# Kernel tuning notes

Measured on AMD Instinct MI355X. Metric: run time of the kernel, lower is better.

Reference implementation:

```python
import jax, jax.numpy as jnp
import numpy as np

N = 50000   # nodes
E = 800000  # edges (avg degree 16)
G = 64      # graphs in batch

def _lin(k, fi, fo):
    kw, kb = jax.random.split(k)
    s = 1.0 / np.sqrt(fi)
    w = jax.random.uniform(kw, (fi, fo), minval=-s, maxval=s, dtype=jnp.float32)
    b = jax.random.uniform(kb, (fo,), minval=-s, maxval=s, dtype=jnp.float32)
    return w, b

def setup_inputs():
    key = jax.random.key(0)
    ks = jax.random.split(key, 12)
    pos = jax.random.normal(ks[0], (N, 3), dtype=jnp.float32)
    edge_index = jax.random.randint(ks[1], (2, E), 0, N, dtype=jnp.int32)
    batch = jnp.sort(jax.random.randint(ks[2], (N,), 0, G, dtype=jnp.int32))
    w_proj, b_proj = _lin(ks[3], 3, 64)
    # message passing layers: self-weight, neighbor-weight, bias
    ws0, bb0 = _lin(ks[4], 64, 64);  wn0, _ = _lin(jax.random.fold_in(ks[4], 1), 64, 64)
    ws1, bb1 = _lin(ks[5], 64, 64);  wn1, _ = _lin(jax.random.fold_in(ks[5], 1), 64, 64)
    ws2, bb2 = _lin(ks[6], 64, 128); wn2, _ = _lin(jax.random.fold_in(ks[6], 1), 64, 128)
    ws3, bb3 = _lin(ks[7], 256, 256); wn3, _ = _lin(jax.random.fold_in(ks[7], 1), 256, 256)
    # dense head: concat(max, mean) = 512 -> 512 -> 256
    wd1, bd1 = _lin(ks[8], 512, 512)
    wd2, bd2 = _lin(ks[9], 512, 256)
    return {"pos": pos, "edge_index": edge_index, "batch": batch,
            "w_proj": w_proj, "b_proj": b_proj,
            "ws0": ws0, "wn0": wn0, "bb0": bb0,
            "ws1": ws1, "wn1": wn1, "bb1": bb1,
            "ws2": ws2, "wn2": wn2, "bb2": bb2,
            "ws3": ws3, "wn3": wn3, "bb3": bb3,
            "wd1": wd1, "bd1": bd1, "wd2": wd2, "bd2": bd2}

def reference(pos, edge_index, batch, w_proj, b_proj,
              ws0, wn0, bb0, ws1, wn1, bb1, ws2, wn2, bb2, ws3, wn3, bb3,
              wd1, bd1, wd2, bd2):
    src, dst = edge_index[0], edge_index[1]
    x = pos @ w_proj + b_proj  # node projection [N,64]
    # in-degree counts, computed once
    deg = jnp.maximum(
        jax.ops.segment_sum(jnp.ones((E, 1), x.dtype), dst, num_segments=N), 1.0)

    def mp(h, ws, wn, b):
        # mean-aggregate neighbor messages: gather on src, scatter-add on dst
        agg = jax.ops.segment_sum(h[src], dst, num_segments=N) / deg
        return jax.nn.leaky_relu(h @ ws + agg @ wn + b)

    h0 = mp(x, ws0, wn0, bb0)   # [N,64]
    h1 = mp(h0, ws1, wn1, bb1)  # [N,64]
    h2 = mp(h1, ws2, wn2, bb2)  # [N,128]
    nf = mp(jnp.concatenate([h0, h1, h2], axis=-1), ws3, wn3, bb3)  # [N,256]

    # scatter max/mean pooling over graph ids
    gcnt = jnp.maximum(
        jax.ops.segment_sum(jnp.ones((N, 1), nf.dtype), batch, num_segments=G), 1.0)
    x1 = jax.ops.segment_max(nf, batch, num_segments=G)
    x2 = jax.ops.segment_sum(nf, batch, num_segments=G) / gcnt
    g = jnp.concatenate([x1, x2], axis=-1)  # [G,512]

    g = jax.nn.leaky_relu(g @ wd1 + bd1)
    return g @ wd2 + bd2  # [G,256]
```

## Files before the change

### kernel.cpp

```cpp
#include <hip/hip_runtime.h>
#include <math.h>

typedef _Float16 f16x8 __attribute__((ext_vector_type(8)));
typedef unsigned short us8 __attribute__((ext_vector_type(8)));
typedef float f32x4 __attribute__((ext_vector_type(4)));

__device__ inline unsigned short f2h(float f) {
    _Float16 h = (_Float16)f;
    return *(unsigned short*)&h;
}
__device__ inline float h2f(unsigned short u) {
    _Float16 h = *(_Float16*)&u;
    return (float)h;
}

__device__ __forceinline__ size_t pkoff(int row, int col, int KT) {
    return ((size_t)(row >> 4) * (KT >> 5) + (col >> 5)) * 512
         + (size_t)(((col >> 3) & 3) * 128 + ((row & 15) << 3) + (col & 7));
}

#define ECH 4096

__global__ __launch_bounds__(256)
void bucket_hist(const int* __restrict__ edst, int* __restrict__ bcnt, int E, int NB) {
    __shared__ int h[512];
    int tid = threadIdx.x;
    for (int i = tid; i < NB; i += 256) h[i] = 0;
    __syncthreads();
    int c0 = blockIdx.x * ECH, c1 = min(c0 + ECH, E);
    for (int e = c0 + tid; e < c1; e += 256) atomicAdd(&h[edst[e] >> 7], 1);
    __syncthreads();
    for (int i = tid; i < NB; i += 256) if (h[i]) atomicAdd(&bcnt[i], h[i]);
}

__global__ __launch_bounds__(512)
void bucket_scan(const int* __restrict__ bcnt, int* __restrict__ bbase,
                 int* __restrict__ bcur, int* __restrict__ rowstart, int NB, int n) {
    __shared__ int ws[8];
    int tid = threadIdx.x, lane = tid & 63, wid = tid >> 6;
    int v = (tid < NB) ? bcnt[tid] : 0;
    int x = v;
    for (int d = 1; d < 64; d <<= 1) { int y = __shfl_up(x, d); if (lane >= d) x += y; }
    if (lane == 63) ws[wid] = x;
    __syncthreads();
    int off = 0;
    for (int w = 0; w < wid; w++) off += ws[w];
    int excl = x - v + off;
    if (tid < NB) { bbase[tid] = excl; bcur[tid] = excl; }
    if (tid == 0) {
        int tot = 0;
        for (int w = 0; w < 8; w++) tot += ws[w];
        bbase[NB] = tot;
        rowstart[n] = tot;
    }
}

__global__ __launch_bounds__(256)
void bucket_scatter(const int* __restrict__ esrc_in, const int* __restrict__ edst_in,
                    int* __restrict__ bcur, unsigned* __restrict__ bedge, int E, int NB) {
    __shared__ int h[512];
    __shared__ int rb[512];
    int tid = threadIdx.x;
    for (int i = tid; i < NB; i += 256) h[i] = 0;
    __syncthreads();
    int c0 = blockIdx.x * ECH, c1 = min(c0 + ECH, E);
    for (int e = c0 + tid; e < c1; e += 256) atomicAdd(&h[edst_in[e] >> 7], 1);
    __syncthreads();
    for (int i = tid; i < NB; i += 256) {
        rb[i] = h[i] ? atomicAdd(&bcur[i], h[i]) : 0;
        h[i] = 0;
    }
    __syncthreads();
    for (int e = c0 + tid; e < c1; e += 256) {
        int dst = edst_in[e], src = esrc_in[e];
        int b = dst >> 7;
        int o = atomicAdd(&h[b], 1);
        bedge[rb[b] + o] = (unsigned)src | ((unsigned)(dst & 127) << 16);
    }
}

__global__ __launch_bounds__(256)
void node_csr(const unsigned* __restrict__ bedge, const int* __restrict__ bbase,
              int* __restrict__ rowstart, float* __restrict__ degf,
              unsigned short* __restrict__ esrc, int n) {
    __shared__ int cnt[128];
    __shared__ int cur[128];
    __shared__ int ws4[4];
    int b = blockIdx.x, tid = threadIdx.x;
    int lane = tid & 63, wid = tid >> 6;
    int n0 = b << 7;
    int eb0 = bbase[b], eb1 = bbase[b + 1];
    if (tid < 128) cnt[tid] = 0;
    __syncthreads();
    for (int e = eb0 + tid; e < eb1; e += 256) atomicAdd(&cnt[(bedge[e] >> 16) & 127], 1);
    __syncthreads();
    int v = (tid < 128) ? cnt[tid] : 0;
    int x = v;
    for (int d = 1; d < 64; d <<= 1) { int y = __shfl_up(x, d); if (lane >= d) x += y; }
    if (lane == 63) ws4[wid] = x;
    __syncthreads();
    int off = 0;
    for (int w = 0; w < wid; w++) off += ws4[w];
    int excl = x - v + off;
    if (tid < 128 && n0 + tid < n) {
        rowstart[n0 + tid] = eb0 + excl;
        cur[tid] = eb0 + excl;
        degf[n0 + tid] = (float)(v > 0 ? v : 1);
    }
    __syncthreads();
    for (int e = eb0 + tid; e < eb1; e += 256) {
        unsigned u = bedge[e];
        int p = atomicAdd(&cur[(u >> 16) & 127], 1);
        esrc[p] = (unsigned short)(u & 0xffffu);
    }
}

__global__ __launch_bounds__(256)
void wcvt_pk(const float* __restrict__ Ws, const float* __restrict__ Wn,
             int K2, int FOUT, unsigned short* __restrict__ out) {
    int t = blockIdx.x * 256 + threadIdx.x;
    int total = 2 * K2 * FOUT;
    if (t >= total) return;
    int k = t / FOUT, n = t - k * FOUT;
    float v = (k < K2) ? Ws[k * FOUT + n] : Wn[(k - K2) * FOUT + n];
    out[pkoff(n, k, 2 * K2)] = f2h(v);
}

__global__ __launch_bounds__(256)
void proj_k(const float* __restrict__ pos, const float* __restrict__ w,
            const float* __restrict__ b, unsigned short* __restrict__ XB0row,
            unsigned short* __restrict__ XB0pk, int n_nodes) {
    int t = blockIdx.x * 256 + threadIdx.x;
    int n = t >> 6, f = t & 63;
    if (n >= n_nodes) return;
    float p0 = pos[n * 3 + 0], p1 = pos[n * 3 + 1], p2 = pos[n * 3 + 2];
    float v = b[f] + p0 * w[f] + p1 * w[64 + f] + p2 * w[128 + f];
    unsigned short h = f2h(v);
    XB0row[(size_t)n * 128 + f] = h;
    XB0pk[pkoff(n, f, 128)] = h;
}

template <int F, int KT>
__global__ __launch_bounds__(256)
void agg_pk(const unsigned short* __restrict__ src, int sstr,
            unsigned short* __restrict__ dpk, int dc,
            const int* __restrict__ rowstart, const unsigned short* __restrict__ esrc,
            const float* __restrict__ degf, int n_nodes) {
    int wave = threadIdx.x >> 6;
    int lane = threadIdx.x & 63;
    int n = blockIdx.x * 4 + wave;
    if (n >= n_nodes) return;
    const int ST = (F == 64) ? 2 : 1;
    int half = (F == 64) ? (lane >> 5) : 0;
    int li   = (F == 64) ? (lane & 31) : lane;
    int e0 = rowstart[n], e1 = rowstart[n + 1];
    float a0 = 0.f, a1 = 0.f;
    int e = e0 + half;
    for (; e + 3 * ST < e1; e += 4 * ST) {
        int s0 = esrc[e], s1 = esrc[e + ST], s2 = esrc[e + 2 * ST], s3 = esrc[e + 3 * ST];
        unsigned p0 = *(const unsigned*)&src[(size_t)s0 * sstr + 2 * li];
        unsigned p1 = *(const unsigned*)&src[(size_t)s1 * sstr + 2 * li];
        unsigned p2 = *(const unsigned*)&src[(size_t)s2 * sstr + 2 * li];
        unsigned p3 = *(const unsigned*)&src[(size_t)s3 * sstr + 2 * li];
        a0 += h2f((unsigned short)(p0 & 0xffffu)) + h2f((unsigned short)(p1 & 0xffffu))
            + h2f((unsigned short)(p2 & 0xffffu)) + h2f((unsigned short)(p3 & 0xffffu));
        a1 += h2f((unsigned short)(p0 >> 16)) + h2f((unsigned short)(p1 >> 16))
            + h2f((unsigned short)(p2 >> 16)) + h2f((unsigned short)(p3 >> 16));
    }
    for (; e < e1; e += ST) {
        int s = esrc[e];
        unsigned p = *(const unsigned*)&src[(size_t)s * sstr + 2 * li];
        a0 += h2f((unsigned short)(p & 0xffffu));
        a1 += h2f((unsigned short)(p >> 16));
    }
    if (F == 64) { a0 += __shfl_xor(a0, 32); a1 += __shfl_xor(a1, 32); }
    float inv = 1.0f / degf[n];
    unsigned out = (unsigned)f2h(a0 * inv) | ((unsigned)f2h(a1 * inv) << 16);
    if (F != 64 || lane < 32) {
        int c = dc + 2 * li;
        *(unsigned*)&dpk[pkoff(n, c, KT)] = out;
    }
}

__device__ inline void atomicMaxFloat(float* addr, float v) {
    if (v >= 0.f) atomicMax((int*)addr, __float_as_int(v));
    else          atomicMin((unsigned int*)addr, __float_as_uint(v));
}

template <int K, int KTA, int MT, int NTB, int POOL>
__global__ __launch_bounds__(64)
void gemm_fr(const unsigned short* __restrict__ Apk, int KA1, int ac1, int ac2,
             const unsigned short* __restrict__ Wpk, const float* __restrict__ bias,
             unsigned short* __restrict__ Drow, int dcol,
             unsigned short* __restrict__ Dpk, int KTD,
             float* __restrict__ pmax, float* __restrict__ psum,
             const int* __restrict__ batch, int M) {
    const int NS = K / 32;
    __shared__ unsigned short tile[MT * 16][NTB * 16 + 8];
    __shared__ int bsh[MT * 16];
    int lane = threadIdx.x;
    int lm = lane & 15, kb = lane >> 4;
    int rb0 = blockIdx.x * MT;
    int nb0 = blockIdx.y * NTB;
    int m0 = rb0 * 16;

    if (POOL) {
        if (lane < MT * 16) {
            int gm = m0 + lane;
            bsh[lane] = batch[gm < M ? gm : (M - 1)];
        }
        __syncthreads();
    }

    f32x4 acc[MT][NTB] = {};

    auto loadf = [&](f16x8* A_, f16x8* B_, int s) {
        int kk = s * 32;
        int phys = (kk < KA1) ? (ac1 + kk) : (ac2 + (kk - KA1));
        size_t ak = (size_t)(phys >> 5) * 512 + (size_t)lane * 8;
        #pragma unroll
        for (int mf = 0; mf < MT; mf++)
            A_[mf] = *(const f16x8*)&Apk[(size_t)(rb0 + mf) * (KTA / 32) * 512 + ak];
        #pragma unroll
        for (int nt = 0; nt < NTB; nt++)
            B_[nt] = *(const f16x8*)&Wpk[((size_t)(nb0 + nt) * (K / 32) + s) * 512 + (size_t)lane * 8];
    };
    auto domfma = [&](f16x8* A_, f16x8* B_) {
        #pragma unroll
        for (int nt = 0; nt < NTB; nt++)
            #pragma unroll
            for (int mf = 0; mf < MT; mf++)
                acc[mf][nt] = __builtin_amdgcn_mfma_f32_16x16x32_f16(A_[mf], B_[nt], acc[mf][nt], 0, 0, 0);
    };

    f16x8 aA[MT], bA[NTB], aB[MT], bB[NTB];
    loadf(aA, bA, 0);
    for (int s = 0; s < NS; s += 2) {
        loadf(aB, bB, s + 1);
        domfma(aA, bA);
        if (s + 2 < NS) loadf(aA, bA, s + 2);
        domfma(aB, bB);
    }

    if (!POOL) {
        #pragma unroll
        for (int nt = 0; nt < NTB; nt++) {
            int colL = nt * 16 + lm;
            float bv = bias[nb0 * 16 + colL];
            #pragma unroll
            for (int mf = 0; mf < MT; mf++) {
                #pragma unroll
                for (int r = 0; r < 4; r++) {
                    float v = acc[mf][nt][r] + bv;
                    v = (v > 0.f) ? v : 0.01f * v;
                    unsigned short h = f2h(v);
                    tile[mf * 16 + kb * 4 + r][colL] = h;
                    int gm = m0 + mf * 16 + kb * 4 + r;
                    if (gm < M) Drow[(size_t)gm * 256 + dcol + nb0 * 16 + colL] = h;
                }
            }
        }
        __syncthreads();
        int dkg0 = (dcol + nb0 * 16) >> 5;
        #pragma unroll
        for (int mf = 0; mf < MT; mf++) {
            #pragma unroll
            for (int kg = 0; kg < NTB / 2; kg++) {
                us8 u = *(const us8*)&tile[mf * 16 + lm][kg * 32 + kb * 8];
                *(us8*)&Dpk[((size_t)(rb0 + mf) * (KTD / 32) + dkg0 + kg) * 512 + (size_t)lane * 8] = u;
            }
        }
    } else {
        bool uni = (bsh[0] == bsh[MT * 16 - 1]);
        if (uni) {
            int g = bsh[0];
            #pragma unroll
            for (int nt = 0; nt < NTB; nt++) {
                int col = (nb0 + nt) * 16 + lm;
                float bv = bias[col];
                float mx = -INFINITY, sm = 0.f;
                #pragma unroll
                for (int mf = 0; mf < MT; mf++) {
                    #pragma unroll
                    for (int r = 0; r < 4; r++) {
                        int gm = m0 + mf * 16 + kb * 4 + r;
                        if (gm >= M) continue;
                        float v = acc[mf][nt][r] + bv;
                        v = (v > 0.f) ? v : 0.01f * v;
                        mx = fmaxf(mx, v); sm += v;
                    }
                }
                mx = fmaxf(mx, __shfl_xor(mx, 16));
                mx = fmaxf(mx, __shfl_xor(mx, 32));
                sm += __shfl_xor(sm, 16);
                sm += __shfl_xor(sm, 32);
                if (kb == 0 && mx > -INFINITY) {
                    atomicMaxFloat(&pmax[g * 256 + col], mx);
                    atomicAdd(&psum[g * 256 + col], sm);
                }
            }
        } else {
            #pragma unroll
            for (int nt = 0; nt < NTB; nt++) {
                int col = (nb0 + nt) * 16 + lm;
                float bv = bias[col];
                int curg = -1; float mx = -INFINITY, sm = 0.f;
                #pragma unroll
                for (int mf = 0; mf < MT; mf++) {
                    #pragma unroll
                    for (int r = 0; r < 4; r++) {
                        int gm = m0 + mf * 16 + kb * 4 + r;
                        if (gm >= M) continue;
                        int g = bsh[mf * 16 + kb * 4 + r];
                        if (g != curg) {
                            if (curg >= 0) {
                                atomicMaxFloat(&pmax[curg * 256 + col], mx);
                                atomicAdd(&psum[curg * 256 + col], sm);
                            }
                            curg = g; mx = -INFINITY; sm = 0.f;
                        }
                        float v = acc[mf][nt][r] + bv;
                        v = (v > 0.f) ? v : 0.01f * v;
                        mx = fmaxf(mx, v); sm += v;
                    }
                }
                if (curg >= 0) {
                    atomicMaxFloat(&pmax[curg * 256 + col], mx);
                    atomicAdd(&psum[curg * 256 + col], sm);
                }
            }
        }
    }
}

template <int K, int FOUT>
__global__ __launch_bounds__(256)
void gemm_lrelu(const float* __restrict__ A1, int a1s, int a1c, int KA1,
                const float* __restrict__ A2, int a2s, int a2c,
                const float* __restrict__ W1, const float* __restrict__ W2,
                const float* __restrict__ bias,
                float* __restrict__ D, int dstr, int dcol, int M, int doRelu) {
    const int BM = 64, BN = 64, BK = 16;
    __shared__ float As[BK][BM];
    __shared__ float Bs[BK][BN];
    int tid = threadIdx.x;
    int m0 = blockIdx.x * BM;
    int n0 = blockIdx.y * BN;
    int tx = tid & 15;
    int ty = tid >> 4;
    float acc[4][4] = {};
    int mA = tid >> 2;
    int kA = (tid & 3) * 4;
    int kB = tid >> 4;
    int nB = (tid & 15) * 4;
    for (int k0 = 0; k0 < K; k0 += BK) {
        int kk = k0 + kA;
        const float* Ap; int Asr; int Acc;
        if (kk < KA1) { Ap = A1; Asr = a1s; Acc = a1c + kk; }
        else          { Ap = A2; Asr = a2s; Acc = a2c + (kk - KA1); }
        int gm = m0 + mA;
        float4 av;
        if (gm < M) av = *(const float4*)&Ap[(size_t)gm * Asr + Acc];
        else        av = float4{0.f, 0.f, 0.f, 0.f};
        As[kA + 0][mA] = av.x; As[kA + 1][mA] = av.y;
        As[kA + 2][mA] = av.z; As[kA + 3][mA] = av.w;
        int kw = k0 + kB;
        const float* Wp; int kwl;
        if (kw < K / 2) { Wp = W1; kwl = kw; } else { Wp = W2; kwl = kw - K / 2; }
        float4 bv = *(const float4*)&Wp[(size_t)kwl * FOUT + n0 + nB];
        *(float4*)&Bs[kB][nB] = bv;
        __syncthreads();
        #pragma unroll
        for (int k = 0; k < BK; k++) {
            float a[4], b[4];
            *(float4*)a = *(const float4*)&As[k][ty * 4];
            *(float4*)b = *(const float4*)&Bs[k][tx * 4];
            #pragma unroll
            for (int i = 0; i < 4; i++)
                #pragma unroll
                for (int j = 0; j < 4; j++)
                    acc[i][j] += a[i] * b[j];
        }
        __syncthreads();
    }
    #pragma unroll
    for (int i = 0; i < 4; i++) {
        int gm = m0 + ty * 4 + i;
        if (gm >= M) continue;
        #pragma unroll
        for (int j = 0; j < 4; j++) {
            int gn = n0 + tx * 4 + j;
            float v = acc[i][j] + bias[gn];
            if (doRelu) v = (v > 0.f) ? v : 0.01f * v;
            D[(size_t)gm * dstr + dcol + gn] = v;
        }
    }
}

__global__ __launch_bounds__(256)
void pool_init(float* __restrict__ pmax, float* __restrict__ psum, int G) {
    int t = blockIdx.x * 256 + threadIdx.x;
    if (t < G * 256) { pmax[t] = -INFINITY; psum[t] = 0.f; }
}

__global__ __launch_bounds__(256)
void pool_final(const float* __restrict__ pmax, const float* __restrict__ psum,
                const int* __restrict__ batch, float* __restrict__ pooled,
                int G, int n_nodes) {
    int t = blockIdx.x * 256 + threadIdx.x;
    if (t >= G * 256) return;
    int g = t >> 8, f = t & 255;
    int lo = 0, hi = n_nodes;
    while (lo < hi) { int mid = (lo + hi) >> 1; if (batch[mid] < g) lo = mid + 1; else hi = mid; }
    int start = lo;
    lo = start; hi = n_nodes;
    while (lo < hi) { int mid = (lo + hi) >> 1; if (batch[mid] < g + 1) lo = mid + 1; else hi = mid; }
    int end = lo;
    int c = end - start;
    float mx = pmax[t];
    if (c == 0) mx = 0.f;
    pooled[g * 512 + f] = mx;
    pooled[g * 512 + 256 + f] = psum[t] / (float)(c > 0 ? c : 1);
}

extern "C" void kernel_launch(void* const* d_in, const int* in_sizes, int n_in,
                              void* d_out, int out_size, void* d_ws, size_t ws_size,
                              hipStream_t stream) {
    const float* pos   = (const float*)d_in[0];
    const int*   eidx  = (const int*)d_in[1];
    const int*   batch = (const int*)d_in[2];
    const float* w_proj = (const float*)d_in[3];
    const float* b_proj = (const float*)d_in[4];
    const float* ws0 = (const float*)d_in[5];  const float* wn0 = (const float*)d_in[6];  const float* bb0 = (const float*)d_in[7];
    const float* ws1 = (const float*)d_in[8];  const float* wn1 = (const float*)d_in[9];  const float* bb1 = (const float*)d_in[10];
    const float* ws2 = (const float*)d_in[11]; const float* wn2 = (const float*)d_in[12]; const float* bb2 = (const float*)d_in[13];
    const float* ws3 = (const float*)d_in[14]; const float* wn3 = (const float*)d_in[15]; const float* bb3 = (const float*)d_in[16];
    const float* wd1 = (const float*)d_in[17]; const float* bd1 = (const float*)d_in[18];
    const float* wd2 = (const float*)d_in[19]; const float* bd2 = (const float*)d_in[20];

    int N = in_sizes[0] / 3;
    int E = in_sizes[1] / 2;
    int G = out_size / 256;
    const int* esrc_in = eidx;
    const int* edst_in = eidx + E;

    int NRB = (N + 15) / 16 + 1;
    int NB  = (N + 127) >> 7;

    char* base = (char*)d_ws;
    size_t off = 0;
    auto alloc = [&](size_t bytes) -> void* {
        void* p = base + off;
        off = (off + bytes + 255) & ~(size_t)255;
        return p;
    };
    int*   rowstart = (int*)alloc((size_t)(N + 1) * 4);
    float* degf     = (float*)alloc((size_t)N * 4);
    int*   bcnt     = (int*)alloc((size_t)512 * 4);
    int*   bbase    = (int*)alloc((size_t)513 * 4);
    int*   bcur     = (int*)alloc((size_t)512 * 4);
    unsigned* bedge = (unsigned*)alloc((size_t)E * 4);
    unsigned short* esrc = (unsigned short*)alloc((size_t)E * 2);
    unsigned short* XB0row = (unsigned short*)alloc((size_t)N * 128 * 2);
    unsigned short* XB0pk  = (unsigned short*)alloc((size_t)NRB * 16 * 128 * 2);
    unsigned short* XBrow  = (unsigned short*)alloc((size_t)N * 256 * 2);
    unsigned short* XBpk   = (unsigned short*)alloc((size_t)NRB * 16 * 512 * 2);
    float* pooled   = (float*)alloc((size_t)G * 512 * 4);
    float* hid      = (float*)alloc((size_t)G * 512 * 4);
    float* pmax     = (float*)alloc((size_t)G * 256 * 4);
    float* psum     = (float*)alloc((size_t)G * 256 * 4);
    unsigned short* WP0 = (unsigned short*)alloc((size_t)64 * 128 * 2);
    unsigned short* WP1 = (unsigned short*)alloc((size_t)64 * 128 * 2);
    unsigned short* WP2 = (unsigned short*)alloc((size_t)128 * 128 * 2);
    unsigned short* WP3 = (unsigned short*)alloc((size_t)256 * 512 * 2);

    wcvt_pk<<<(2 * 64 * 64 + 255) / 256, 256, 0, stream>>>(ws0, wn0, 64, 64, WP0);
    wcvt_pk<<<(2 * 64 * 64 + 255) / 256, 256, 0, stream>>>(ws1, wn1, 64, 64, WP1);
    wcvt_pk<<<(2 * 64 * 128 + 255) / 256, 256, 0, stream>>>(ws2, wn2, 64, 128, WP2);
    wcvt_pk<<<(2 * 256 * 256 + 255) / 256, 256, 0, stream>>>(ws3, wn3, 256, 256, WP3);

    (void)hipMemsetAsync(bcnt, 0, (size_t)512 * 4, stream);
    int eb = (E + ECH - 1) / ECH;
    bucket_hist<<<eb, 256, 0, stream>>>(edst_in, bcnt, E, NB);
    bucket_scan<<<1, 512, 0, stream>>>(bcnt, bbase, bcur, rowstart, NB, N);
    bucket_scatter<<<eb, 256, 0, stream>>>(esrc_in, edst_in, bcur, bedge, E, NB);
    node_csr<<<NB, 256, 0, stream>>>(bedge, bbase, rowstart, degf, esrc, N);

    proj_k<<<(N * 64 + 255) / 256, 256, 0, stream>>>(pos, w_proj, b_proj, XB0row, XB0pk, N);

    int ab = (N + 3) / 4;
    int gb = (N + 31) / 32;

    agg_pk<64, 128><<<ab, 256, 0, stream>>>(XB0row, 128, XB0pk, 64, rowstart, esrc, degf, N);
    gemm_fr<128, 128, 2, 4, 0><<<dim3(gb, 1), 64, 0, stream>>>(
        XB0pk, 128, 0, 0, WP0, bb0, XBrow, 0, XBpk, 512, nullptr, nullptr, nullptr, N);

    agg_pk<64, 512><<<ab, 256, 0, stream>>>(XBrow, 256, XBpk, 256, rowstart, esrc, degf, N);
    gemm_fr<128, 512, 2, 4, 0><<<dim3(gb, 1), 64, 0, stream>>>(
        XBpk, 64, 0, 256, WP1, bb1, XBrow, 64, XBpk, 512, nullptr, nullptr, nullptr, N);

    agg_pk<64, 512><<<ab, 256, 0, stream>>>(XBrow + 64, 256, XBpk, 320, rowstart, esrc, degf, N);
    gemm_fr<128, 512, 2, 4, 0><<<dim3(gb, 2), 64, 0, stream>>>(
        XBpk, 64, 64, 320, WP2, bb2, XBrow, 128, XBpk, 512, nullptr, nullptr, nullptr, N);

    agg_pk<128, 512><<<ab, 256, 0, stream>>>(XBrow + 128, 256, XBpk, 384, rowstart, esrc, degf, N);
    pool_init<<<(G * 256 + 255) / 256, 256, 0, stream>>>(pmax, psum, G);
    gemm_fr<512, 512, 2, 8, 1><<<dim3(gb, 2), 64, 0, stream>>>(
        XBpk, 512, 0, 0, WP3, bb3, nullptr, 0, nullptr, 512, pmax, psum, batch, N);
    pool_final<<<(G * 256 + 255) / 256, 256, 0, stream>>>(pmax, psum, batch, pooled, G, N);

    gemm_lrelu<512, 512><<<dim3((G + 63) / 64, 8), 256, 0, stream>>>(
        pooled, 512, 0, 512, pooled, 512, 0, wd1, wd1 + 256 * 512, bd1, hid, 512, 0, G, 1);
    gemm_lrelu<512, 256><<<dim3((G + 63) / 64, 4), 256, 0, stream>>>(
        hid, 512, 0, 512, hid, 512, 0, wd2, wd2 + 256 * 256, bd2, (float*)d_out, 256, 0, G, 0);
}
```

Baseline: 319.6 us.

## Pack four waves per GEMM block and deepen A-fragment prefetch pipeline

The fragment GEMM now runs four independent wavefronts per 256-thread block, each taking its own 32-row stripe with a private LDS tile, so no block-wide barriers are needed. The K loop is fully unrolled with a 6-deep register ring buffer for A fragments and a 2-deep one for B, so more global loads are in flight ahead of the MFMAs. The pooling variant reads batch ids straight from global memory instead of staging them in shared memory. Register pressure rises with the deeper buffers and could reduce occupancy, and the padded row-block count grows to cover the larger grid granularity.

```diff
diff --git a/kernel.cpp b/kernel.cpp
--- a/kernel.cpp
+++ b/kernel.cpp
@@ -188,7 +188,7 @@
 }
 
 template <int K, int KTA, int MT, int NTB, int POOL>
-__global__ __launch_bounds__(64)
+__global__ __launch_bounds__(256)
 void gemm_fr(const unsigned short* __restrict__ Apk, int KA1, int ac1, int ac2,
              const unsigned short* __restrict__ Wpk, const float* __restrict__ bias,
              unsigned short* __restrict__ Drow, int dcol,
@@ -196,50 +196,52 @@
              float* __restrict__ pmax, float* __restrict__ psum,
              const int* __restrict__ batch, int M) {
     const int NS = K / 32;
-    __shared__ unsigned short tile[MT * 16][NTB * 16 + 8];
-    __shared__ int bsh[MT * 16];
-    int lane = threadIdx.x;
+    const int AD = (NS < 6) ? NS : 6;
+    const int BD = (NS < 2) ? NS : 2;
+    const int TSZ = POOL ? 4 : (MT * 16) * (NTB * 16 + 8);
+    __shared__ unsigned short tile_s[4][TSZ];
+    int w = threadIdx.x >> 6;
+    int lane = threadIdx.x & 63;
     int lm = lane & 15, kb = lane >> 4;
-    int rb0 = blockIdx.x * MT;
+    int rb0 = (blockIdx.x * 4 + w) * MT;
     int nb0 = blockIdx.y * NTB;
     int m0 = rb0 * 16;
-
-    if (POOL) {
-        if (lane < MT * 16) {
-            int gm = m0 + lane;
-            bsh[lane] = batch[gm < M ? gm : (M - 1)];
-        }
-        __syncthreads();
-    }
+    if (m0 >= M) return;
+    unsigned short* tile = tile_s[w];
 
     f32x4 acc[MT][NTB] = {};
-
-    auto loadf = [&](f16x8* A_, f16x8* B_, int s) {
+    f16x8 Ab[AD][MT];
+    f16x8 Bb[BD][NTB];
+
+    auto loadA = [&](int slot, int s) {
         int kk = s * 32;
         int phys = (kk < KA1) ? (ac1 + kk) : (ac2 + (kk - KA1));
         size_t ak = (size_t)(phys >> 5) * 512 + (size_t)lane * 8;
         #pragma unroll
         for (int mf = 0; mf < MT; mf++)
-            A_[mf] = *(const f16x8*)&Apk[(size_t)(rb0 + mf) * (KTA / 32) * 512 + ak];
+            Ab[slot][mf] = *(const f16x8*)&Apk[(size_t)(rb0 + mf) * (KTA / 32) * 512 + ak];
+    };
+    auto loadB = [&](int slot, int s) {
         #pragma unroll
         for (int nt = 0; nt < NTB; nt++)
-            B_[nt] = *(const f16x8*)&Wpk[((size_t)(nb0 + nt) * (K / 32) + s) * 512 + (size_t)lane * 8];
+            Bb[slot][nt] = *(const f16x8*)&Wpk[((size_t)(nb0 + nt) * (K / 32) + s) * 512 + (size_t)lane * 8];
     };
-    auto domfma = [&](f16x8* A_, f16x8* B_) {
+
+    #pragma unroll
+    for (int p = 0; p < AD; p++) loadA(p, p);
+    #pragma unroll
+    for (int p = 0; p < BD; p++) loadB(p, p);
+
+    #pragma unroll
+    for (int s = 0; s < NS; s++) {
         #pragma unroll
         for (int nt = 0; nt < NTB; nt++)
             #pragma unroll
             for (int mf = 0; mf < MT; mf++)
-                acc[mf][nt] = __builtin_amdgcn_mfma_f32_16x16x32_f16(A_[mf], B_[nt], acc[mf][nt], 0, 0, 0);
-    };
-
-    f16x8 aA[MT], bA[NTB], aB[MT], bB[NTB];
-    loadf(aA, bA, 0);
-    for (int s = 0; s < NS; s += 2) {
-        loadf(aB, bB, s + 1);
-        domfma(aA, bA);
-        if (s + 2 < NS) loadf(aA, bA, s + 2);
-        domfma(aB, bB);
+                acc[mf][nt] = __builtin_amdgcn_mfma_f32_16x16x32_f16(
+                    Ab[s % AD][mf], Bb[s % BD][nt], acc[mf][nt], 0, 0, 0);
+        if (s + BD < NS) loadB(s % BD, s + BD);
+        if (s + AD < NS) loadA(s % AD, s + AD);
     }
 
     if (!POOL) {
@@ -254,26 +256,34 @@
                     float v = acc[mf][nt][r] + bv;
                     v = (v > 0.f) ? v : 0.01f * v;
                     unsigned short h = f2h(v);
-                    tile[mf * 16 + kb * 4 + r][colL] = h;
+                    tile[(mf * 16 + kb * 4 + r) * (NTB * 16 + 8) + colL] = h;
                     int gm = m0 + mf * 16 + kb * 4 + r;
                     if (gm < M) Drow[(size_t)gm * 256 + dcol + nb0 * 16 + colL] = h;
                 }
             }
         }
-        __syncthreads();
         int dkg0 = (dcol + nb0 * 16) >> 5;
         #pragma unroll
         for (int mf = 0; mf < MT; mf++) {
             #pragma unroll
             for (int kg = 0; kg < NTB / 2; kg++) {
-                us8 u = *(const us8*)&tile[mf * 16 + lm][kg * 32 + kb * 8];
+                us8 u = *(const us8*)&tile[(mf * 16 + lm) * (NTB * 16 + 8) + kg * 32 + kb * 8];
                 *(us8*)&Dpk[((size_t)(rb0 + mf) * (KTD / 32) + dkg0 + kg) * 512 + (size_t)lane * 8] = u;
             }
         }
     } else {
-        bool uni = (bsh[0] == bsh[MT * 16 - 1]);
+        int grow[MT * 4];
+        #pragma unroll
+        for (int mf = 0; mf < MT; mf++)
+            #pragma unroll
+            for (int r = 0; r < 4; r++) {
+                int gm = m0 + mf * 16 + kb * 4 + r;
+                grow[mf * 4 + r] = batch[gm < M ? gm : (M - 1)];
+            }
+        int mlast = m0 + MT * 16 - 1;
+        bool uni = (batch[m0] == batch[mlast < M ? mlast : (M - 1)]);
         if (uni) {
-            int g = bsh[0];
+            int g = grow[0];
             #pragma unroll
             for (int nt = 0; nt < NTB; nt++) {
                 int col = (nb0 + nt) * 16 + lm;
@@ -311,7 +321,7 @@
                     for (int r = 0; r < 4; r++) {
                         int gm = m0 + mf * 16 + kb * 4 + r;
                         if (gm >= M) continue;
-                        int g = bsh[mf * 16 + kb * 4 + r];
+                        int g = grow[mf * 4 + r];
                         if (g != curg) {
                             if (curg >= 0) {
                                 atomicMaxFloat(&pmax[curg * 256 + col], mx);
@@ -444,7 +454,8 @@
     const int* esrc_in = eidx;
     const int* edst_in = eidx + E;
 
-    int NRB = (N + 15) / 16 + 1;
+    int gbx = (N + 127) / 128;
+    int NRB = gbx * 8 + 8;
     int NB  = (N + 127) >> 7;
 
     char* base = (char*)d_ws;
@@ -489,23 +500,22 @@
     proj_k<<<(N * 64 + 255) / 256, 256, 0, stream>>>(pos, w_proj, b_proj, XB0row, XB0pk, N);
 
     int ab = (N + 3) / 4;
-    int gb = (N + 31) / 32;
 
     agg_pk<64, 128><<<ab, 256, 0, stream>>>(XB0row, 128, XB0pk, 64, rowstart, esrc, degf, N);
-    gemm_fr<128, 128, 2, 4, 0><<<dim3(gb, 1), 64, 0, stream>>>(
+    gemm_fr<128, 128, 2, 4, 0><<<dim3(gbx, 1), 256, 0, stream>>>(
         XB0pk, 128, 0, 0, WP0, bb0, XBrow, 0, XBpk, 512, nullptr, nullptr, nullptr, N);
 
     agg_pk<64, 512><<<ab, 256, 0, stream>>>(XBrow, 256, XBpk, 256, rowstart, esrc, degf, N);
-    gemm_fr<128, 512, 2, 4, 0><<<dim3(gb, 1), 64, 0, stream>>>(
+    gemm_fr<128, 512, 2, 4, 0><<<dim3(gbx, 1), 256, 0, stream>>>(
         XBpk, 64, 0, 256, WP1, bb1, XBrow, 64, XBpk, 512, nullptr, nullptr, nullptr, N);
 
     agg_pk<64, 512><<<ab, 256, 0, stream>>>(XBrow + 64, 256, XBpk, 320, rowstart, esrc, degf, N);
-    gemm_fr<128, 512, 2, 4, 0><<<dim3(gb, 2), 64, 0, stream>>>(
+    gemm_fr<128, 512, 2, 4, 0><<<dim3(gbx, 2), 256, 0, stream>>>(
         XBpk, 64, 64, 320, WP2, bb2, XBrow, 128, XBpk, 512, nullptr, nullptr, nullptr, N);
 
     agg_pk<128, 512><<<ab, 256, 0, stream>>>(XBrow + 128, 256, XBpk, 384, rowstart, esrc, degf, N);
     pool_init<<<(G * 256 + 255) / 256, 256, 0, stream>>>(pmax, psum, G);
-    gemm_fr<512, 512, 2, 8, 1><<<dim3(gb, 2), 64, 0, stream>>>(
+    gemm_fr<512, 512, 2, 8, 1><<<dim3(gbx, 2), 256, 0, stream>>>(
         XBpk, 512, 0, 0, WP3, bb3, nullptr, 0, nullptr, 512, pmax, psum, batch, N);
     pool_final<<<(G * 256 + 255) / 256, 256, 0, stream>>>(pmax, psum, batch, pooled, G, N);
 
```

After: 359.6 us. 1.13x slower.
